# Kernel tuning notes

Hardware: AMD Instinct MI355X
Metric: run time of the kernel (lower is better)

The kernel has to match this reference:

```python
import jax, jax.numpy as jnp
import numpy as np


def _nearest(img, cy, cx):
    # PyTorch F.grid_sample(mode='nearest', align_corners=False, padding_mode='zeros').
    # img: [B,C,H,W]; cy,cx: [B,N] normalized coords in [-1,1] (cy->H axis, cx->W axis).
    B, C, H, W = img.shape
    iy = jnp.rint((cy + 1.0) * H / 2.0 - 0.5)  # unnormalize then nearbyint
    ix = jnp.rint((cx + 1.0) * W / 2.0 - 0.5)
    valid = (iy >= 0) & (iy < H) & (ix >= 0) & (ix < W)
    flat = (jnp.clip(iy, 0, H - 1).astype(jnp.int32) * W
            + jnp.clip(ix, 0, W - 1).astype(jnp.int32))  # [B,N]
    g = jnp.take_along_axis(img.reshape(B, C, H * W), flat[:, None, :], axis=2)  # [B,C,N]
    g = jnp.where(valid[:, None, :], g, 0.0)
    return g.transpose(0, 2, 1)  # [B,N,C]


def setup_inputs() -> dict:
    key = jax.random.key(0)
    ks = jax.random.split(key, 16)
    B, N = 2, 16384
    h, w = 64, 64       # LR feat / lr_guide resolution
    H, W = 256, 256     # HR guide resolution
    Cf, Cg = 128, 128   # feat_dim, guide_dim
    inp = {
        'feat': jax.random.normal(ks[0], (B, Cf, h, w), jnp.float32),
        'coord': jax.random.uniform(ks[1], (B, N, 2), jnp.float32) * 2.0 - 1.0,
        'hr_guide': jax.random.normal(ks[2], (B, Cg, H, W), jnp.float32),
        'lr_guide': jax.random.normal(ks[3], (B, Cg, h, w), jnp.float32),
    }
    dims = [386, 1024, 512, 256, 128, 2]  # imnet_in_dim -> hidden_list -> out_dim
    for i in range(5):
        fan_in, fan_out = dims[i], dims[i + 1]
        scale = np.sqrt(2.0 / fan_in).astype(np.float32)
        inp[f'W{i}'] = jax.random.normal(ks[4 + i], (fan_out, fan_in), jnp.float32) * scale
        inp[f'b{i}'] = jnp.zeros((fan_out,), jnp.float32)
    return inp


def reference(feat, coord, hr_guide, lr_guide, W0, b0, W1, b1, W2, b2, W3, b3, W4, b4):
    b, c, h, w = feat.shape
    # make_coord((h,w), flatten=False).permute(2,0,1): channel 0 = y (h axis), 1 = x (w axis)
    ys = -1.0 + 2.0 * (jnp.arange(h, dtype=jnp.float32) + 0.5) / h
    xs = -1.0 + 2.0 * (jnp.arange(w, dtype=jnp.float32) + 0.5) / w
    fc = jnp.stack([jnp.broadcast_to(ys[:, None], (h, w)),
                    jnp.broadcast_to(xs[None, :], (h, w))], 0)[None]  # [1,2,h,w]
    fc = jnp.broadcast_to(fc, (b, 2, h, w))

    # coord.flip(-1) as grid -> grid x = coord[...,1] (W axis), grid y = coord[...,0] (H axis)
    q_guide_hr = _nearest(hr_guide, coord[..., 0], coord[..., 1])  # [B,N,Cg]

    # 4 offsets (vx,vy) in [-1,1]x[-1,1], scaled by rx=1/h, ry=1/w (loop order of torch code)
    offs = jnp.array([[-1., -1.], [-1., 1.], [1., -1.], [1., 1.]], jnp.float32)
    offs = offs * jnp.array([1.0 / h, 1.0 / w], jnp.float32)
    cK = coord[None] + offs[:, None, None, :]  # [4,B,N,2]

    samp = jax.vmap(_nearest, in_axes=(None, 0, 0))
    q_feat = samp(feat, cK[..., 0], cK[..., 1])      # [4,B,N,Cf]
    q_coord = samp(fc, cK[..., 0], cK[..., 1])       # [4,B,N,2]
    q_lr = samp(lr_guide, cK[..., 0], cK[..., 1])    # [4,B,N,Cg]

    rel = (coord[None] - q_coord) * jnp.array([float(h), float(w)], jnp.float32)  # [4,B,N,2]
    qg_hr = jnp.broadcast_to(q_guide_hr[None], q_lr.shape)
    inp = jnp.concatenate([q_feat, qg_hr, qg_hr - q_lr, rel], axis=-1)  # [4,B,N,386]

    x = inp
    for Wl, bl in ((W0, b0), (W1, b1), (W2, b2), (W3, b3)):
        x = jax.nn.relu(x @ Wl.T + bl)
    preds = x @ W4.T + b4                      # [4,B,N,2]
    preds = jnp.moveaxis(preds, 0, -1)         # [B,N,2,4]
    wgt = jax.nn.softmax(preds[:, :, 1, :], axis=-1)
    return jnp.sum(preds[:, :, 0, :] * wgt, axis=-1, keepdims=True)  # [B,N,1]
```

## Files before the change

### kernel.cpp

```cpp
#include <hip/hip_runtime.h>
#include <cstdint>

typedef unsigned short u16;
typedef __attribute__((ext_vector_type(8))) _Float16 half8;
typedef __attribute__((ext_vector_type(4))) float    f32x4;

#define BN 2
#define NN 16384
#define FH 64
#define FW 64
#define GH 256
#define GW 256
#define CC 128
#define K0P 416
#define M_TOTAL (4*BN*NN)
#define MROWS 64
#define NBLK (M_TOTAL/MROWS)

#define SX 424
#define SB 520
#define S3 264
#define S4 136
#define OB (MROWS*SX)
#define LDS_ELEMS (OB + MROWS*SB)

__device__ __forceinline__ half8 zero8() {
  half8 z;
#pragma unroll
  for (int e = 0; e < 8; ++e) z[e] = (_Float16)0.f;
  return z;
}

__global__ void pack_w(const float* __restrict__ w, _Float16* __restrict__ out,
                       int NOUT, int K, int KT) {
  int idx = blockIdx.x * 256 + threadIdx.x;
  int total = (NOUT / 16) * KT * 64;
  if (idx >= total) return;
  int l = idx & 63;
  int t = idx >> 6;
  int kt = t % KT;
  int jt = t / KT;
  int row = jt * 16 + (l & 15);
  int k0 = kt * 32 + (l >> 4) * 8;
  _Float16* o = out + (size_t)idx * 8;
#pragma unroll
  for (int e = 0; e < 8; ++e) {
    int k = k0 + e;
    float v = (k < K) ? w[(size_t)row * K + k] : 0.f;
    o[e] = (_Float16)v;
  }
}

__global__ void transpose_to_hwc(const float* __restrict__ in, _Float16* __restrict__ out,
                                 int C, int HH, int WW) {
  __shared__ float tile[32][33];
  const int xt = blockIdx.x, ct = blockIdx.y;
  const int bb = blockIdx.z / HH, y = blockIdx.z % HH;
  const int tx = threadIdx.x, ty = threadIdx.y;
  const int x0 = xt * 32, c0 = ct * 32;
#pragma unroll
  for (int i = 0; i < 4; ++i) {
    int c = c0 + ty + i * 8;
    tile[ty + i * 8][tx] = in[((size_t)(bb * C + c) * HH + y) * WW + x0 + tx];
  }
  __syncthreads();
#pragma unroll
  for (int i = 0; i < 4; ++i) {
    int x = x0 + ty + i * 8;
    out[((size_t)(bb * HH + y) * WW + x) * C + c0 + tx] = (_Float16)tile[tx][ty + i * 8];
  }
}

template<int KT, int JT>
__device__ __forceinline__ void gemm_block(f32x4 (*acc)[4],
    const _Float16* lin, int ldi,
    const _Float16* __restrict__ Wt, int wTileStride,
    int lane) {
  const int lr = lane & 15, lk = (lane >> 4) * 8;
#pragma unroll 2
  for (int kt = 0; kt < KT; ++kt) {
    half8 B[JT];
#pragma unroll
    for (int jj = 0; jj < JT; ++jj)
      B[jj] = *(const half8*)(Wt + (size_t)jj * wTileStride + (kt * 64 + lane) * 8);
    half8 A[4];
#pragma unroll
    for (int rt = 0; rt < 4; ++rt)
      A[rt] = *(const half8*)(lin + (rt * 16 + lr) * ldi + kt * 32 + lk);
#pragma unroll
    for (int jj = 0; jj < JT; ++jj)
#pragma unroll
      for (int rt = 0; rt < 4; ++rt)
        acc[jj][rt] = __builtin_amdgcn_mfma_f32_16x16x32_f16(A[rt], B[jj], acc[jj][rt], 0, 0, 0);
  }
}

template<int JT, bool RELU>
__device__ __forceinline__ void store_h(const f32x4 (*acc)[4], _Float16* lout, int ldo,
                                        int colbase, const float* __restrict__ bias, int lane) {
  const int lr = lane & 15, rhi = (lane >> 4) * 4;
#pragma unroll
  for (int jj = 0; jj < JT; ++jj) {
    const int col = colbase + jj * 16 + lr;
    const float bv = bias[col];
#pragma unroll
    for (int rt = 0; rt < 4; ++rt)
#pragma unroll
      for (int rr = 0; rr < 4; ++rr) {
        float v = acc[jj][rt][rr] + bv;
        if (RELU) v = fmaxf(v, 0.f);
        lout[(rt * 16 + rhi + rr) * ldo + col] = (_Float16)v;
      }
  }
}

__global__ __launch_bounds__(512, 2) void jiif_main(
    const float* __restrict__ coord,
    const _Float16* __restrict__ featT, const _Float16* __restrict__ hrT,
    const _Float16* __restrict__ lrT,
    const _Float16* __restrict__ W0p, const _Float16* __restrict__ W1p,
    const _Float16* __restrict__ W2p, const _Float16* __restrict__ W3p,
    const float* __restrict__ b0, const float* __restrict__ b1,
    const float* __restrict__ b2, const float* __restrict__ b3,
    const float* __restrict__ W4, const float* __restrict__ b4,
    float* __restrict__ preds) {
  extern __shared__ _Float16 lds[];
  const int tid = threadIdx.x;
  const int wave = tid >> 6, lane = tid & 63;
  const int m0 = blockIdx.x * MROWS;
  _Float16* X  = lds;
  _Float16* Hb = lds + OB;

  {
    const int r = tid >> 3;
    const int g = tid & 7;
    const int row = m0 + r;
    const int n = row & (NN - 1);
    const int bb = (row >> 14) & (BN - 1);
    const int k = row >> 15;
    const float c0 = coord[((size_t)bb * NN + n) * 2 + 0];
    const float c1 = coord[((size_t)bb * NN + n) * 2 + 1];
    const float cy = c0 + ((k < 2) ? -1.f : 1.f) * (1.f / FH);
    const float cx = c1 + ((k & 1) ? 1.f : -1.f) * (1.f / FW);
    const float fy = rintf((cy + 1.f) * (FH * 0.5f) - 0.5f);
    const float fx = rintf((cx + 1.f) * (FW * 0.5f) - 0.5f);
    const bool vF = (fy >= 0.f) && (fy < (float)FH) && (fx >= 0.f) && (fx < (float)FW);
    const int iy = max(0, min(FH - 1, (int)fy));
    const int ix = max(0, min(FW - 1, (int)fx));
    const float gy = rintf((c0 + 1.f) * (GH * 0.5f) - 0.5f);
    const float gx = rintf((c1 + 1.f) * (GW * 0.5f) - 0.5f);
    const bool vH = (gy >= 0.f) && (gy < (float)GH) && (gx >= 0.f) && (gx < (float)GW);
    const int jy = max(0, min(GH - 1, (int)gy));
    const int jx = max(0, min(GW - 1, (int)gx));
    const _Float16* fp = featT + (size_t)((bb * FH + iy) * FW + ix) * CC;
    const _Float16* lp = lrT  + (size_t)((bb * FH + iy) * FW + ix) * CC;
    const _Float16* hp = hrT  + (size_t)((bb * GH + jy) * GW + jx) * CC;
    _Float16* xr = X + r * SX;
#pragma unroll
    for (int t = 0; t < 2; ++t) {
      const int c8 = g * 16 + t * 8;
      half8 fv = vF ? *(const half8*)(fp + c8) : zero8();
      half8 lv = vF ? *(const half8*)(lp + c8) : zero8();
      half8 hv = vH ? *(const half8*)(hp + c8) : zero8();
      *(half8*)(xr + c8) = fv;
      *(half8*)(xr + CC + c8) = hv;
      half8 dv = hv - lv;
      *(half8*)(xr + 2 * CC + c8) = dv;
    }
    if (g == 0) {
      const float qc0 = vF ? (-1.f + (float)(2 * iy + 1) * (1.f / FH)) : 0.f;
      const float qc1 = vF ? (-1.f + (float)(2 * ix + 1) * (1.f / FW)) : 0.f;
      xr[384] = (_Float16)((c0 - qc0) * (float)FH);
      xr[385] = (_Float16)((c1 - qc1) * (float)FW);
#pragma unroll
      for (int c = 386; c < K0P; ++c) xr[c] = (_Float16)0.f;
    }
  }
  __syncthreads();

  f32x4 acc2[4][4];
#pragma unroll
  for (int a = 0; a < 4; ++a)
#pragma unroll
    for (int b = 0; b < 4; ++b) acc2[a][b] = (f32x4){0.f, 0.f, 0.f, 0.f};

#pragma unroll 1
  for (int p = 0; p < 2; ++p) {
    f32x4 acc0[4][4];
#pragma unroll
    for (int a = 0; a < 4; ++a)
#pragma unroll
      for (int b = 0; b < 4; ++b) acc0[a][b] = (f32x4){0.f, 0.f, 0.f, 0.f};
    gemm_block<13, 4>(acc0, X, SX, W0p + (size_t)(p * 32 + wave * 4) * 13 * 512, 13 * 512, lane);
    store_h<4, true>(acc0, Hb, SB, wave * 64, b0 + p * 512, lane);
    __syncthreads();
    gemm_block<16, 4>(acc2, Hb, SB,
                      W1p + (size_t)(wave * 4) * 32 * 512 + (size_t)(p * 16) * 512, 32 * 512, lane);
    __syncthreads();
  }
  store_h<4, true>(acc2, Hb, SB, wave * 64, b1, lane);
  __syncthreads();

  {
    f32x4 acc3[2][4];
#pragma unroll
    for (int a = 0; a < 2; ++a)
#pragma unroll
      for (int b = 0; b < 4; ++b) acc3[a][b] = (f32x4){0.f, 0.f, 0.f, 0.f};
    gemm_block<16, 2>(acc3, Hb, SB, W2p + (size_t)(wave * 2) * 16 * 512, 16 * 512, lane);
    __syncthreads();
    store_h<2, true>(acc3, X, S3, wave * 32, b2, lane);
    __syncthreads();
  }

  {
    f32x4 acc4[1][4];
#pragma unroll
    for (int b = 0; b < 4; ++b) acc4[0][b] = (f32x4){0.f, 0.f, 0.f, 0.f};
    gemm_block<8, 1>(acc4, X, S3, W3p + (size_t)wave * 8 * 512, 8 * 512, lane);
    __syncthreads();
    store_h<1, true>(acc4, Hb, S4, wave * 16, b3, lane);
    __syncthreads();
  }

  {
    const int m = tid >> 3;
    const int sub = tid & 7;
    const int j = sub & 1;
    const int q = sub >> 1;
    const _Float16* h4 = Hb + m * S4 + q * 32;
    const float* w4 = W4 + j * CC + q * 32;
    float s = 0.f;
#pragma unroll
    for (int c = 0; c < 32; ++c) s += (float)h4[c] * w4[c];
    s += __shfl_xor(s, 2);
    s += __shfl_xor(s, 4);
    if (q == 0) preds[(size_t)(m0 + m) * 2 + j] = s + b4[j];
  }
}

__global__ void jiif_combine(const float* __restrict__ preds, float* __restrict__ out) {
  const int i = blockIdx.x * 256 + threadIdx.x;
  if (i >= BN * NN) return;
  float p0[4], p1[4];
#pragma unroll
  for (int k = 0; k < 4; ++k) {
    p0[k] = preds[((size_t)k * BN * NN + i) * 2 + 0];
    p1[k] = preds[((size_t)k * BN * NN + i) * 2 + 1];
  }
  float mx = fmaxf(fmaxf(p1[0], p1[1]), fmaxf(p1[2], p1[3]));
  float se = 0.f, so = 0.f;
#pragma unroll
  for (int k = 0; k < 4; ++k) {
    float e = expf(p1[k] - mx);
    se += e;
    so += p0[k] * e;
  }
  out[i] = so / se;
}

extern "C" void kernel_launch(void* const* d_in, const int* in_sizes, int n_in,
                              void* d_out, int out_size, void* d_ws, size_t ws_size,
                              hipStream_t stream) {
  const float* feat  = (const float*)d_in[0];
  const float* coord = (const float*)d_in[1];
  const float* hr    = (const float*)d_in[2];
  const float* lr    = (const float*)d_in[3];
  const float* W0 = (const float*)d_in[4];  const float* b0 = (const float*)d_in[5];
  const float* W1 = (const float*)d_in[6];  const float* b1 = (const float*)d_in[7];
  const float* W2 = (const float*)d_in[8];  const float* b2 = (const float*)d_in[9];
  const float* W3 = (const float*)d_in[10]; const float* b3 = (const float*)d_in[11];
  const float* W4 = (const float*)d_in[12]; const float* b4 = (const float*)d_in[13];

  char* ws = (char*)d_ws;
  _Float16* W0p   = (_Float16*)(ws + 0);
  _Float16* W1p   = (_Float16*)(ws + 851968);
  _Float16* W2p   = (_Float16*)(ws + 1900544);
  _Float16* W3p   = (_Float16*)(ws + 2162688);
  _Float16* featT = (_Float16*)(ws + 2228224);
  _Float16* hrT   = (_Float16*)(ws + 4325376);
  _Float16* lrT   = (_Float16*)(ws + 37879808);
  float* preds    = (float*)(ws + 39976960);
  if (ws_size < 41025536) return;

  pack_w<<<208, 256, 0, stream>>>(W0, W0p, 1024, 386, 13);
  pack_w<<<256, 256, 0, stream>>>(W1, W1p, 512, 1024, 32);
  pack_w<<<64,  256, 0, stream>>>(W2, W2p, 256, 512, 16);
  pack_w<<<16,  256, 0, stream>>>(W3, W3p, 128, 256, 8);

  transpose_to_hwc<<<dim3(2, 4, 128), dim3(32, 8), 0, stream>>>(feat, featT, CC, FH, FW);
  transpose_to_hwc<<<dim3(8, 4, 512), dim3(32, 8), 0, stream>>>(hr,   hrT,   CC, GH, GW);
  transpose_to_hwc<<<dim3(2, 4, 128), dim3(32, 8), 0, stream>>>(lr,   lrT,   CC, FH, FW);

  (void)hipFuncSetAttribute((const void*)jiif_main,
                            hipFuncAttributeMaxDynamicSharedMemorySize, LDS_ELEMS * 2);
  jiif_main<<<NBLK, 512, LDS_ELEMS * 2, stream>>>(
      coord, featT, hrT, lrT, W0p, W1p, W2p, W3p, b0, b1, b2, b3, W4, b4, preds);

  jiif_combine<<<(BN * NN + 255) / 256, 256, 0, stream>>>(preds, (float*)d_out);
}
```

Baseline: 371.5 us.

## Switch MLP to 32x32x16 MFMA with chunked layer fusion and smaller LDS

The main MLP kernel moves from 16x16x32 to 32x32x16 f16 MFMA tiles, with weights repacked to match and weights fed as the A operand. Layer 0 output is now computed in 128-column chunks that are consumed immediately by layer 1. This shrinks the intermediate LDS buffer and lets the launch bound rise to 4 blocks per CU. Later layers reuse aliased LDS regions and store with packed 64-bit writes. The cost is more block barriers per chunk and heavier register pressure from the 16-wide accumulators.

Measured after the change: 377.3 us. Within noise of the previous version (+1.6%).

```diff
diff --git a/kernel.cpp b/kernel.cpp
--- a/kernel.cpp
+++ b/kernel.cpp
@@ -1,9 +1,8 @@
 #include <hip/hip_runtime.h>
 #include <cstdint>
 
-typedef unsigned short u16;
 typedef __attribute__((ext_vector_type(8))) _Float16 half8;
-typedef __attribute__((ext_vector_type(4))) float    f32x4;
+typedef __attribute__((ext_vector_type(16))) float   f32x16;
 
 #define BN 2
 #define NN 16384
@@ -12,41 +11,49 @@
 #define GH 256
 #define GW 256
 #define CC 128
-#define K0P 416
 #define M_TOTAL (4*BN*NN)
 #define MROWS 64
 #define NBLK (M_TOTAL/MROWS)
 
 #define SX 424
-#define SB 520
-#define S3 264
+#define SC 136
+#define S2 264
 #define S4 136
-#define OB (MROWS*SX)
-#define LDS_ELEMS (OB + MROWS*SB)
-
-__device__ __forceinline__ half8 zero8() {
+#define OFF_HC 27136
+#define OFF_H3 16896
+#define LDS_ELEMS 35840
+
+#define MFMA(a,b,c) __builtin_amdgcn_mfma_f32_32x32x16_f16((a),(b),(c),0,0,0)
+
+static __device__ __forceinline__ f32x16 zero16() {
+  f32x16 z;
+#pragma unroll
+  for (int i = 0; i < 16; ++i) z[i] = 0.f;
+  return z;
+}
+static __device__ __forceinline__ half8 zero8() {
   half8 z;
 #pragma unroll
   for (int e = 0; e < 8; ++e) z[e] = (_Float16)0.f;
   return z;
 }
 
-__global__ void pack_w(const float* __restrict__ w, _Float16* __restrict__ out,
-                       int NOUT, int K, int KT) {
+__global__ void pack_w(const float* __restrict__ wsrc, _Float16* __restrict__ out,
+                       int NT, int K, int KT) {
   int idx = blockIdx.x * 256 + threadIdx.x;
-  int total = (NOUT / 16) * KT * 64;
+  int total = NT * KT * 64;
   if (idx >= total) return;
   int l = idx & 63;
   int t = idx >> 6;
   int kt = t % KT;
   int jt = t / KT;
-  int row = jt * 16 + (l & 15);
-  int k0 = kt * 32 + (l >> 4) * 8;
+  int row = jt * 32 + (l & 31);
+  int k0 = kt * 16 + (l >> 5) * 8;
   _Float16* o = out + (size_t)idx * 8;
 #pragma unroll
   for (int e = 0; e < 8; ++e) {
     int k = k0 + e;
-    float v = (k < K) ? w[(size_t)row * K + k] : 0.f;
+    float v = (k < K) ? wsrc[(size_t)row * K + k] : 0.f;
     o[e] = (_Float16)v;
   }
 }
@@ -71,50 +78,29 @@
   }
 }
 
-template<int KT, int JT>
-__device__ __forceinline__ void gemm_block(f32x4 (*acc)[4],
-    const _Float16* lin, int ldi,
-    const _Float16* __restrict__ Wt, int wTileStride,
-    int lane) {
-  const int lr = lane & 15, lk = (lane >> 4) * 8;
-#pragma unroll 2
-  for (int kt = 0; kt < KT; ++kt) {
-    half8 B[JT];
-#pragma unroll
-    for (int jj = 0; jj < JT; ++jj)
-      B[jj] = *(const half8*)(Wt + (size_t)jj * wTileStride + (kt * 64 + lane) * 8);
-    half8 A[4];
-#pragma unroll
-    for (int rt = 0; rt < 4; ++rt)
-      A[rt] = *(const half8*)(lin + (rt * 16 + lr) * ldi + kt * 32 + lk);
-#pragma unroll
-    for (int jj = 0; jj < JT; ++jj)
-#pragma unroll
-      for (int rt = 0; rt < 4; ++rt)
-        acc[jj][rt] = __builtin_amdgcn_mfma_f32_16x16x32_f16(A[rt], B[jj], acc[jj][rt], 0, 0, 0);
-  }
-}
-
-template<int JT, bool RELU>
-__device__ __forceinline__ void store_h(const f32x4 (*acc)[4], _Float16* lout, int ldo,
-                                        int colbase, const float* __restrict__ bias, int lane) {
-  const int lr = lane & 15, rhi = (lane >> 4) * 4;
-#pragma unroll
-  for (int jj = 0; jj < JT; ++jj) {
-    const int col = colbase + jj * 16 + lr;
-    const float bv = bias[col];
-#pragma unroll
-    for (int rt = 0; rt < 4; ++rt)
-#pragma unroll
-      for (int rr = 0; rr < 4; ++rr) {
-        float v = acc[jj][rt][rr] + bv;
-        if (RELU) v = fmaxf(v, 0.f);
-        lout[(rt * 16 + rhi + rr) * ldo + col] = (_Float16)v;
-      }
-  }
-}
-
-__global__ __launch_bounds__(512, 2) void jiif_main(
+template<bool RELU>
+static __device__ __forceinline__ void store_tile(const f32x16 acc, _Float16* lout, int ldo,
+                                                  int row0, int col0,
+                                                  const float* __restrict__ biasBase, int lane) {
+  const int m = row0 + (lane & 31);
+  const int s4 = (lane >> 5) * 4;
+  _Float16* rp = lout + (size_t)m * ldo + col0 + s4;
+  const float* bp = biasBase + s4;
+#pragma unroll
+  for (int g = 0; g < 4; ++g) {
+    float4 bv = *(const float4*)(bp + 8 * g);
+    union { _Float16 h[4]; unsigned long long u; } pk;
+#pragma unroll
+    for (int e = 0; e < 4; ++e) {
+      float v = acc[4 * g + e] + ((const float*)&bv)[e];
+      if (RELU) v = fmaxf(v, 0.f);
+      pk.h[e] = (_Float16)v;
+    }
+    *(unsigned long long*)(rp + 8 * g) = pk.u;
+  }
+}
+
+__global__ __launch_bounds__(512, 4) void jiif_main(
     const float* __restrict__ coord,
     const _Float16* __restrict__ featT, const _Float16* __restrict__ hrT,
     const _Float16* __restrict__ lrT,
@@ -126,10 +112,13 @@
     float* __restrict__ preds) {
   extern __shared__ _Float16 lds[];
   const int tid = threadIdx.x;
-  const int wave = tid >> 6, lane = tid & 63;
+  const int w = tid >> 6, lane = tid & 63;
   const int m0 = blockIdx.x * MROWS;
-  _Float16* X  = lds;
-  _Float16* Hb = lds + OB;
+  _Float16* X   = lds;
+  _Float16* Hc  = lds + OFF_HC;
+  _Float16* H2r = lds;
+  _Float16* H3r = lds + OFF_H3;
+  _Float16* H4r = lds;
 
   {
     const int r = tid >> 3;
@@ -155,7 +144,7 @@
     const _Float16* fp = featT + (size_t)((bb * FH + iy) * FW + ix) * CC;
     const _Float16* lp = lrT  + (size_t)((bb * FH + iy) * FW + ix) * CC;
     const _Float16* hp = hrT  + (size_t)((bb * GH + jy) * GW + jx) * CC;
-    _Float16* xr = X + r * SX;
+    _Float16* xr = X + (size_t)r * SX;
 #pragma unroll
     for (int t = 0; t < 2; ++t) {
       const int c8 = g * 16 + t * 8;
@@ -173,66 +162,116 @@
       xr[384] = (_Float16)((c0 - qc0) * (float)FH);
       xr[385] = (_Float16)((c1 - qc1) * (float)FW);
 #pragma unroll
-      for (int c = 386; c < K0P; ++c) xr[c] = (_Float16)0.f;
-    }
-  }
-  __syncthreads();
-
-  f32x4 acc2[4][4];
-#pragma unroll
-  for (int a = 0; a < 4; ++a)
-#pragma unroll
-    for (int b = 0; b < 4; ++b) acc2[a][b] = (f32x4){0.f, 0.f, 0.f, 0.f};
-
+      for (int c = 386; c < 416; ++c) xr[c] = (_Float16)0.f;
+    }
+  }
+  __syncthreads();
+
+  const int m31 = lane & 31;
+  const int s8 = (lane >> 5) * 8;
+  const int mt = w & 1;
+  const int jl = w >> 1;
+
+  f32x16 a2_00 = zero16(), a2_01 = zero16(), a2_10 = zero16(), a2_11 = zero16();
 #pragma unroll 1
-  for (int p = 0; p < 2; ++p) {
-    f32x4 acc0[4][4];
-#pragma unroll
-    for (int a = 0; a < 4; ++a)
-#pragma unroll
-      for (int b = 0; b < 4; ++b) acc0[a][b] = (f32x4){0.f, 0.f, 0.f, 0.f};
-    gemm_block<13, 4>(acc0, X, SX, W0p + (size_t)(p * 32 + wave * 4) * 13 * 512, 13 * 512, lane);
-    store_h<4, true>(acc0, Hb, SB, wave * 64, b0 + p * 512, lane);
+  for (int c = 0; c < 8; ++c) {
+    f32x16 a0 = zero16();
+    {
+      const _Float16* xb = X + (size_t)(mt * 32 + m31) * SX + s8;
+      const _Float16* wb = W0p + ((size_t)((c * 4 + jl) * 26) * 64 + lane) * 8;
+#pragma unroll 2
+      for (int kt = 0; kt < 26; ++kt) {
+        half8 A = *(const half8*)(wb + kt * 512);
+        half8 B = *(const half8*)(xb + kt * 16);
+        a0 = MFMA(A, B, a0);
+      }
+    }
+    store_tile<true>(a0, Hc, SC, mt * 32, jl * 32, b0 + c * 128 + jl * 32, lane);
     __syncthreads();
-    gemm_block<16, 4>(acc2, Hb, SB,
-                      W1p + (size_t)(wave * 4) * 32 * 512 + (size_t)(p * 16) * 512, 32 * 512, lane);
+    {
+      const _Float16* hb0 = Hc + (size_t)m31 * SC + s8;
+      const _Float16* hb1 = Hc + (size_t)(32 + m31) * SC + s8;
+      const _Float16* w1a = W1p + ((size_t)(w * 64 + c * 8) * 64 + lane) * 8;
+      const _Float16* w1b = W1p + ((size_t)((w + 8) * 64 + c * 8) * 64 + lane) * 8;
+#pragma unroll 2
+      for (int kt = 0; kt < 8; ++kt) {
+        half8 A0 = *(const half8*)(w1a + kt * 512);
+        half8 A1 = *(const half8*)(w1b + kt * 512);
+        half8 B0 = *(const half8*)(hb0 + kt * 16);
+        half8 B1 = *(const half8*)(hb1 + kt * 16);
+        a2_00 = MFMA(A0, B0, a2_00);
+        a2_01 = MFMA(A0, B1, a2_01);
+        a2_10 = MFMA(A1, B0, a2_10);
+        a2_11 = MFMA(A1, B1, a2_11);
+      }
+    }
     __syncthreads();
   }
-  store_h<4, true>(acc2, Hb, SB, wave * 64, b1, lane);
-  __syncthreads();
-
-  {
-    f32x4 acc3[2][4];
-#pragma unroll
-    for (int a = 0; a < 2; ++a)
-#pragma unroll
-      for (int b = 0; b < 4; ++b) acc3[a][b] = (f32x4){0.f, 0.f, 0.f, 0.f};
-    gemm_block<16, 2>(acc3, Hb, SB, W2p + (size_t)(wave * 2) * 16 * 512, 16 * 512, lane);
-    __syncthreads();
-    store_h<2, true>(acc3, X, S3, wave * 32, b2, lane);
-    __syncthreads();
-  }
-
-  {
-    f32x4 acc4[1][4];
-#pragma unroll
-    for (int b = 0; b < 4; ++b) acc4[0][b] = (f32x4){0.f, 0.f, 0.f, 0.f};
-    gemm_block<8, 1>(acc4, X, S3, W3p + (size_t)wave * 8 * 512, 8 * 512, lane);
-    __syncthreads();
-    store_h<1, true>(acc4, Hb, S4, wave * 16, b3, lane);
-    __syncthreads();
-  }
+
+  f32x16 a3a = zero16(), a3b = zero16();
+  const int j2a = w >> 1, j2b = (w >> 1) + 4;
+  store_tile<true>(a2_00, H2r, S2, 0,  w * 32, b1 + w * 32, lane);
+  store_tile<true>(a2_01, H2r, S2, 32, w * 32, b1 + w * 32, lane);
+  __syncthreads();
+  {
+    const _Float16* hb = H2r + (size_t)(mt * 32 + m31) * S2 + s8;
+    const _Float16* wa = W2p + ((size_t)(j2a * 32) * 64 + lane) * 8;
+    const _Float16* wb2 = W2p + ((size_t)(j2b * 32) * 64 + lane) * 8;
+#pragma unroll 2
+    for (int kt = 0; kt < 16; ++kt) {
+      half8 A0 = *(const half8*)(wa + kt * 512);
+      half8 A1 = *(const half8*)(wb2 + kt * 512);
+      half8 B = *(const half8*)(hb + kt * 16);
+      a3a = MFMA(A0, B, a3a);
+      a3b = MFMA(A1, B, a3b);
+    }
+  }
+  __syncthreads();
+  store_tile<true>(a2_10, H2r, S2, 0,  w * 32, b1 + 256 + w * 32, lane);
+  store_tile<true>(a2_11, H2r, S2, 32, w * 32, b1 + 256 + w * 32, lane);
+  __syncthreads();
+  {
+    const _Float16* hb = H2r + (size_t)(mt * 32 + m31) * S2 + s8;
+    const _Float16* wa = W2p + ((size_t)(j2a * 32 + 16) * 64 + lane) * 8;
+    const _Float16* wb2 = W2p + ((size_t)(j2b * 32 + 16) * 64 + lane) * 8;
+#pragma unroll 2
+    for (int kt = 0; kt < 16; ++kt) {
+      half8 A0 = *(const half8*)(wa + kt * 512);
+      half8 A1 = *(const half8*)(wb2 + kt * 512);
+      half8 B = *(const half8*)(hb + kt * 16);
+      a3a = MFMA(A0, B, a3a);
+      a3b = MFMA(A1, B, a3b);
+    }
+  }
+  store_tile<true>(a3a, H3r, S2, mt * 32, j2a * 32, b2 + j2a * 32, lane);
+  store_tile<true>(a3b, H3r, S2, mt * 32, j2b * 32, b2 + j2b * 32, lane);
+  __syncthreads();
+
+  {
+    const int j3 = w >> 1;
+    f32x16 a4 = zero16();
+    const _Float16* hb = H3r + (size_t)(mt * 32 + m31) * S2 + s8;
+    const _Float16* wb3 = W3p + ((size_t)(j3 * 16) * 64 + lane) * 8;
+#pragma unroll 2
+    for (int kt = 0; kt < 16; ++kt) {
+      half8 A = *(const half8*)(wb3 + kt * 512);
+      half8 B = *(const half8*)(hb + kt * 16);
+      a4 = MFMA(A, B, a4);
+    }
+    store_tile<true>(a4, H4r, S4, mt * 32, j3 * 32, b3 + j3 * 32, lane);
+  }
+  __syncthreads();
 
   {
     const int m = tid >> 3;
     const int sub = tid & 7;
     const int j = sub & 1;
     const int q = sub >> 1;
-    const _Float16* h4 = Hb + m * S4 + q * 32;
+    const _Float16* h4 = H4r + (size_t)m * S4 + q * 32;
     const float* w4 = W4 + j * CC + q * 32;
     float s = 0.f;
 #pragma unroll
-    for (int c = 0; c < 32; ++c) s += (float)h4[c] * w4[c];
+    for (int cc = 0; cc < 32; ++cc) s += (float)h4[cc] * w4[cc];
     s += __shfl_xor(s, 2);
     s += __shfl_xor(s, 4);
     if (q == 0) preds[(size_t)(m0 + m) * 2 + j] = s + b4[j];
@@ -283,10 +322,10 @@
   float* preds    = (float*)(ws + 39976960);
   if (ws_size < 41025536) return;
 
-  pack_w<<<208, 256, 0, stream>>>(W0, W0p, 1024, 386, 13);
-  pack_w<<<256, 256, 0, stream>>>(W1, W1p, 512, 1024, 32);
-  pack_w<<<64,  256, 0, stream>>>(W2, W2p, 256, 512, 16);
-  pack_w<<<16,  256, 0, stream>>>(W3, W3p, 128, 256, 8);
+  pack_w<<<208, 256, 0, stream>>>(W0, W0p, 32, 386, 26);
+  pack_w<<<256, 256, 0, stream>>>(W1, W1p, 16, 1024, 64);
+  pack_w<<<64,  256, 0, stream>>>(W2, W2p, 8, 512, 32);
+  pack_w<<<16,  256, 0, stream>>>(W3, W3p, 4, 256, 16);
 
   transpose_to_hwc<<<dim3(2, 4, 128), dim3(32, 8), 0, stream>>>(feat, featT, CC, FH, FW);
   transpose_to_hwc<<<dim3(8, 4, 512), dim3(32, 8), 0, stream>>>(hr,   hrT,   CC, GH, GW);
```
